# Kernel optimization log

Measured on AMD Instinct MI355X. Metric: run time of the kernel, lower is better.

Reference implementation:

```python
import jax, jax.numpy as jnp
import numpy as np

INV3 = 1.0 / np.sqrt(3.0)


def setup_inputs() -> dict:
    key = jax.random.key(0)
    ks = jax.random.split(key, 16)
    N, E = 50000, 800000
    inp = {
        'node_input': jax.random.normal(ks[0], (N, 160), jnp.float32),
        'node_attr': jnp.ones((N, 1), jnp.float32),
        'edge_attr': jax.random.normal(ks[1], (E, 4), jnp.float32),
        'edge_scalars': jax.random.normal(ks[2], (E, 8), jnp.float32),
        # params (e3nn internal weights ~ N(0,1))
        'sc_w0': jax.random.normal(ks[3], (64, 64), jnp.float32),
        'sc_w1': jax.random.normal(ks[4], (32, 32), jnp.float32),
        'lin1_w0': jax.random.normal(ks[5], (64, 64), jnp.float32),
        'lin1_w1': jax.random.normal(ks[6], (32, 32), jnp.float32),
        'fc_w1': jax.random.normal(ks[7], (8, 64), jnp.float32),
        'fc_w2': jax.random.normal(ks[8], (64, 192), jnp.float32),
        'lin2_w0': jax.random.normal(ks[9], (96, 64), jnp.float32),
        'lin2_w1': jax.random.normal(ks[10], (96, 32), jnp.float32),
        'lin3_w': jax.random.normal(ks[11], (96, 1), jnp.float32),
        'edge_src': jax.random.randint(ks[12], (E,), 0, N),
        'edge_dst': jax.random.randint(ks[13], (E,), 0, N),
        'num_neighbors': 16,
    }
    return inp


def _fctp(x_s, x_v, attr, w0, w1):
    # FullyConnectedTensorProduct(irreps, '0e', irreps-like): per-irrep linear * scalar attr,
    # path-normalized by 1/sqrt(fan_in mul)
    s = (x_s @ w0) * (1.0 / np.sqrt(x_s.shape[-1])) * attr
    v = jnp.einsum('nud,uw->nwd', x_v, w1) * (1.0 / np.sqrt(x_v.shape[-2])) * attr[..., None]
    return s, v


def reference(node_input, node_attr, edge_attr, edge_scalars,
              sc_w0, sc_w1, lin1_w0, lin1_w1, fc_w1, fc_w2,
              lin2_w0, lin2_w1, lin3_w, edge_src, edge_dst, num_neighbors):
    N = node_input.shape[0]
    # radial MLP -> per-edge TP weights [E, 192]
    h = jax.nn.silu(edge_scalars @ fc_w1 * (1.0 / np.sqrt(8.0)))
    weight = (h @ fc_w2) * (1.0 / np.sqrt(64.0))

    xs, xv = node_input[:, :64], node_input[:, 64:].reshape(N, 32, 3)  # 64x0e, 32x1o
    sc_s, sc_v = _fctp(xs, xv, node_attr, sc_w0, sc_w1)       # self connection
    f_s, f_v = _fctp(xs, xv, node_attr, lin1_w0, lin1_w1)     # lin1

    gs = f_s[edge_src]                 # [E,64]
    gv = f_v[edge_src]                 # [E,32,3]
    ys, yv = edge_attr[:, :1], edge_attr[:, 1:]  # SH 0e, 1o
    w1_, w2_ = weight[:, :64], weight[:, 64:128]
    w3_, w4_ = weight[:, 128:160], weight[:, 160:192]
    # uvu tensor-product paths (component-normalized CG)
    m0a = gs * ys * w1_                                        # 0e x 0e -> 64x0e
    m0b = jnp.sum(gv * yv[:, None, :], -1) * INV3 * w4_        # 1o x 1o -> 32x0e
    m1a = gs[..., None] * yv[:, None, :] * w2_[..., None]      # 0e x 1o -> 64x1o
    m1b = gv * ys[..., None] * w3_[..., None]                  # 1o x 0e -> 32x1o
    E = m0a.shape[0]
    edge_feat = jnp.concatenate(
        [m0a, m0b, m1a.reshape(E, 192), m1b.reshape(E, 96)], -1)  # [E,384] mid layout

    mid = jax.ops.segment_sum(edge_feat, edge_dst, num_segments=N)
    mid = mid / np.sqrt(float(num_neighbors))
    mid_s, mid_v = mid[:, :96], mid[:, 96:].reshape(N, 96, 3)

    c_s, c_v = _fctp(mid_s, mid_v, node_attr, lin2_w0, lin2_w1)
    conv = jnp.concatenate([c_s, c_v.reshape(N, -1)], -1)
    scfeat = jnp.concatenate([sc_s, sc_v.reshape(N, -1)], -1)

    angle = 0.1 * (mid_s @ lin3_w) * (1.0 / np.sqrt(96.0)) * node_attr  # [N,1]
    # sc.output_mask is all-ones here (every output irrep has a path), so sin unchanged
    return jnp.cos(angle) * scfeat + jnp.sin(angle) * conv
```

## Files before the change

kernel.cpp:

```cpp
#include <hip/hip_runtime.h>
#include <math.h>

#define INV3 0.57735026918962576f
#define RS8  0.35355339059327373f
#define RS32 0.17677669529663687f
#define RS64 0.125f
#define RS96 0.10206207261596575f
#define CAP  96

typedef _Float16 v8h   __attribute__((ext_vector_type(8)));
typedef float    f32x4 __attribute__((ext_vector_type(4)));

__global__ void node_prep(const float* __restrict__ node_input,
                          const float* __restrict__ node_attr,
                          const float* __restrict__ w0,
                          const float* __restrict__ w1,
                          float* __restrict__ f, int N) {
    int n = blockIdx.x;
    if (n >= N) return;
    __shared__ float x[160];
    int t = threadIdx.x;
    for (int i = t; i < 160; i += 64) x[i] = node_input[(size_t)n * 160 + i];
    __syncthreads();
    float attr = node_attr[n];
    float acc = 0.f;
    #pragma unroll 8
    for (int i = 0; i < 64; ++i) acc += x[i] * w0[i * 64 + t];
    f[(size_t)n * 160 + t] = acc * RS64 * attr;
    for (int o = t; o < 96; o += 64) {
        int w = o / 3, d = o % 3;
        float a = 0.f;
        #pragma unroll 8
        for (int u = 0; u < 32; ++u) a += x[64 + u * 3 + d] * w1[u * 32 + w];
        f[(size_t)n * 160 + 64 + o] = a * RS32 * attr;
    }
}

__global__ void fill_csr(const int* __restrict__ edge_dst, int* __restrict__ deg,
                         int* __restrict__ bucket, int E) {
    int e = blockIdx.x * blockDim.x + threadIdx.x;
    if (e >= E) return;
    int d = edge_dst[e];
    int pos = atomicAdd(&deg[d], 1);
    if (pos < CAP) bucket[(size_t)d * CAP + pos] = e;
}

__global__ void swizzle_w2(const float* __restrict__ fc_w2, _Float16* __restrict__ Bsw) {
    int idx = blockIdx.x * blockDim.x + threadIdx.x;
    if (idx >= 12288) return;
    int j = idx & 7;
    int l = (idx >> 3) & 63;
    int q = (idx >> 9) & 1;
    int t = idx >> 10;
    int k = q * 32 + ((l >> 4) * 8) + j;
    int n = t * 16 + (l & 15);
    Bsw[idx] = (_Float16)(fc_w2[k * 192 + n] * RS64);
}

__global__ __launch_bounds__(64, 4) void node_main(
    const float* __restrict__ node_input,
    const float* __restrict__ node_attr,
    const float* __restrict__ edge_attr,
    const float* __restrict__ edge_scalars,
    const float* __restrict__ fc_w1,
    const float* __restrict__ f,
    const _Float16* __restrict__ Bsw_g,
    const int* __restrict__ deg,
    const int* __restrict__ bucket,
    const int* __restrict__ edge_src,
    const float* __restrict__ sc_w0,
    const float* __restrict__ sc_w1,
    const float* __restrict__ lin2_w0,
    const float* __restrict__ lin2_w1,
    const float* __restrict__ lin3_w,
    const int* __restrict__ num_neighbors,
    float* __restrict__ out, int N)
{
    __shared__ __align__(16) _Float16 Hl[1024];
    __shared__ __align__(16) _Float16 Wl[16 * 208];
    __shared__ __align__(16) float    ES[16][8];
    __shared__ __align__(16) float    EA[16][4];
    __shared__ int SRC[16];

    const int lane = threadIdx.x;
    const int n    = blockIdx.x;
    if (n >= N) return;

    float fw1[8];
    #pragma unroll
    for (int u = 0; u < 8; ++u) fw1[u] = fc_w1[u * 64 + lane];

    int deg_n = min(deg[n], CAP);
    int nch = (deg_n + 15) >> 4;

    float a0 = 0.f, a1x = 0.f, a1y = 0.f, a1z = 0.f;
    float a2x = 0.f, a2y = 0.f, a2z = 0.f;
    const int m16  = lane & 15;
    const int quad = lane >> 4;
    const int wv   = lane & 31;

    for (int ch = 0; ch < nch; ++ch) {
        int vcnt = deg_n - ch * 16;
        vcnt = vcnt > 16 ? 16 : vcnt;

        if (lane < 16) {
            int i = lane;
            if (i < vcnt) {
                int e = bucket[(size_t)n * CAP + ch * 16 + i];
                SRC[i] = edge_src[e];
                *(float4*)&EA[i][0] = ((const float4*)edge_attr)[e];
                *(float4*)&ES[i][0] = ((const float4*)edge_scalars)[2 * e];
                *(float4*)&ES[i][4] = ((const float4*)edge_scalars)[2 * e + 1];
            } else {
                float4 z = make_float4(0.f, 0.f, 0.f, 0.f);
                SRC[i] = 0;
                *(float4*)&EA[i][0] = z;
                *(float4*)&ES[i][0] = z;
                *(float4*)&ES[i][4] = z;
            }
        }
        __syncthreads();

        #pragma unroll 4
        for (int i = 0; i < 16; ++i) {
            float4 e0 = *(const float4*)&ES[i][0];
            float4 e1 = *(const float4*)&ES[i][4];
            float acc = e0.x * fw1[0] + e0.y * fw1[1] + e0.z * fw1[2] + e0.w * fw1[3]
                      + e1.x * fw1[4] + e1.y * fw1[5] + e1.z * fw1[6] + e1.w * fw1[7];
            acc *= RS8;
            float hh = acc / (1.f + __expf(-acc));
            Hl[i * 64 + lane] = (_Float16)hh;
        }
        __syncthreads();

        v8h A0 = *(const v8h*)&Hl[m16 * 64 + quad * 8];
        v8h A1 = *(const v8h*)&Hl[m16 * 64 + 32 + quad * 8];
        #pragma unroll
        for (int t = 0; t < 12; ++t) {
            v8h B0 = *(const v8h*)&Bsw_g[(2 * t + 0) * 512 + lane * 8];
            v8h B1 = *(const v8h*)&Bsw_g[(2 * t + 1) * 512 + lane * 8];
            f32x4 c = {0.f, 0.f, 0.f, 0.f};
            c = __builtin_amdgcn_mfma_f32_16x16x32_f16(A0, B0, c, 0, 0, 0);
            c = __builtin_amdgcn_mfma_f32_16x16x32_f16(A1, B1, c, 0, 0, 0);
            #pragma unroll
            for (int r = 0; r < 4; ++r)
                Wl[(quad * 4 + r) * 208 + t * 16 + m16] = (_Float16)c[r];
        }
        __syncthreads();

        for (int i0 = 0; i0 < vcnt; i0 += 4) {
            float W0v[4], W1v[4], W2v[4];
            float4 eav[4];
            const float* fsv[4];
            #pragma unroll
            for (int j = 0; j < 4; ++j) {
                int i = i0 + j;
                W0v[j] = (float)Wl[i * 208 + lane];
                W1v[j] = (float)Wl[i * 208 + 64 + lane];
                W2v[j] = (float)Wl[i * 208 + 128 + lane];
                eav[j] = *(const float4*)&EA[i][0];
                fsv[j] = f + (size_t)SRC[i] * 160;
            }
            float gsv[4], g0v[4], g1v[4], g2v[4];
            #pragma unroll
            for (int j = 0; j < 4; ++j) {
                gsv[j] = fsv[j][lane];
                g0v[j] = fsv[j][64 + wv * 3 + 0];
                g1v[j] = fsv[j][64 + wv * 3 + 1];
                g2v[j] = fsv[j][64 + wv * 3 + 2];
            }
            #pragma unroll
            for (int j = 0; j < 4; ++j) {
                float4 ea = eav[j];
                a0 += gsv[j] * ea.x * W0v[j];
                float gW1 = gsv[j] * W1v[j];
                a1x += gW1 * ea.y; a1y += gW1 * ea.z; a1z += gW1 * ea.w;
                if (lane < 32) {
                    float t2 = ea.x * W2v[j];
                    a2x += g0v[j] * t2; a2y += g1v[j] * t2; a2z += g2v[j] * t2;
                } else {
                    a2x += (g0v[j] * ea.y + g1v[j] * ea.z + g2v[j] * ea.w)
                           * (INV3 * W2v[j]);
                }
            }
        }
        __syncthreads();
    }

    float* M = (float*)&Wl[0];
    float* X = (float*)&Hl[0];
    float rs = rsqrtf((float)num_neighbors[0]);
    M[lane] = a0 * rs;
    M[96 + lane * 3 + 0] = a1x * rs;
    M[96 + lane * 3 + 1] = a1y * rs;
    M[96 + lane * 3 + 2] = a1z * rs;
    if (lane < 32) {
        M[288 + lane * 3 + 0] = a2x * rs;
        M[288 + lane * 3 + 1] = a2y * rs;
        M[288 + lane * 3 + 2] = a2z * rs;
    } else {
        M[64 + (lane - 32)] = a2x * rs;
    }
    for (int i = lane; i < 160; i += 64) X[i] = node_input[(size_t)n * 160 + i];
    __syncthreads();

    float attr = node_attr[n];
    float ang = 0.f;
    #pragma unroll 8
    for (int u = 0; u < 96; ++u) ang += M[u] * lin3_w[u];
    ang *= 0.1f * RS96 * attr;
    float ca = cosf(ang), sa = sinf(ang);

    float cs = 0.f;
    #pragma unroll 8
    for (int u = 0; u < 96; ++u) cs += M[u] * lin2_w0[u * 64 + lane];
    cs *= RS96 * attr;
    float ss = 0.f;
    #pragma unroll 8
    for (int i2 = 0; i2 < 64; ++i2) ss += X[i2] * sc_w0[i2 * 64 + lane];
    ss *= RS64 * attr;
    out[(size_t)n * 160 + lane] = ca * ss + sa * cs;

    for (int o = lane; o < 96; o += 64) {
        int ww = o / 3, d = o % 3;
        float cv = 0.f;
        #pragma unroll 8
        for (int u = 0; u < 96; ++u) cv += M[96 + u * 3 + d] * lin2_w1[u * 32 + ww];
        cv *= RS96 * attr;
        float sv = 0.f;
        #pragma unroll 8
        for (int u = 0; u < 32; ++u) sv += X[64 + u * 3 + d] * sc_w1[u * 32 + ww];
        sv *= RS32 * attr;
        out[(size_t)n * 160 + 64 + o] = ca * sv + sa * cv;
    }
}

extern "C" void kernel_launch(void* const* d_in, const int* in_sizes, int n_in,
                              void* d_out, int out_size, void* d_ws, size_t ws_size,
                              hipStream_t stream) {
    const float* node_input   = (const float*)d_in[0];
    const float* node_attr    = (const float*)d_in[1];
    const float* edge_attr    = (const float*)d_in[2];
    const float* edge_scalars = (const float*)d_in[3];
    const float* sc_w0        = (const float*)d_in[4];
    const float* sc_w1        = (const float*)d_in[5];
    const float* lin1_w0      = (const float*)d_in[6];
    const float* lin1_w1      = (const float*)d_in[7];
    const float* fc_w1        = (const float*)d_in[8];
    const float* fc_w2        = (const float*)d_in[9];
    const float* lin2_w0      = (const float*)d_in[10];
    const float* lin2_w1      = (const float*)d_in[11];
    const float* lin3_w       = (const float*)d_in[12];
    const int*   edge_src     = (const int*)d_in[13];
    const int*   edge_dst     = (const int*)d_in[14];
    const int*   num_neigh    = (const int*)d_in[15];

    int N = in_sizes[0] / 160;
    int E = in_sizes[13];

    char* ws = (char*)d_ws;
    size_t off = 0;
    float* f = (float*)(ws + off);            off += ((size_t)N * 160 * 4 + 255) & ~(size_t)255;
    int* deg = (int*)(ws + off);              off += ((size_t)N * 4 + 255) & ~(size_t)255;
    int* bucket = (int*)(ws + off);           off += ((size_t)N * CAP * 4 + 255) & ~(size_t)255;
    _Float16* Bsw_g = (_Float16*)(ws + off);  off += (12288 * 2 + 255) & ~(size_t)255;

    hipMemsetAsync(deg, 0, (size_t)N * sizeof(int), stream);

    fill_csr<<<(E + 255) / 256, 256, 0, stream>>>(edge_dst, deg, bucket, E);
    swizzle_w2<<<48, 256, 0, stream>>>(fc_w2, Bsw_g);
    node_prep<<<N, 64, 0, stream>>>(node_input, node_attr, lin1_w0, lin1_w1, f, N);

    node_main<<<N, 64, 0, stream>>>(
        node_input, node_attr, edge_attr, edge_scalars, fc_w1, f, Bsw_g,
        deg, bucket, edge_src, sc_w0, sc_w1, lin2_w0, lin2_w1, lin3_w,
        num_neigh, (float*)d_out, N);
}
```

Baseline: 768.5 us.

## Batch node linear layers on MFMA and split epilogue into separate kernel

Replaces the per-node scalar linear layers (lin1 prep, and the lin2/sc/lin3 epilogue) with kernels that process 16 nodes per block using fp16 MFMA. A single swizzle kernel pre-packs all weight matrices and folds the normalization constants into them. node_main now writes fp16 mid features to a workspace buffer, which the new final kernel reads. Source-feature gathers for all 16 edges are issued before the radial MLP so their latency can overlap with it, and the per-node edge cap drops from 96 to 64. The trade-off is lower precision from fp16 inputs and the stored fp16 mid features, an extra global round-trip for mid, and a lower degree cap.

```diff
diff --git a/kernel.cpp b/kernel.cpp
--- a/kernel.cpp
+++ b/kernel.cpp
@@ -6,34 +6,49 @@
 #define RS32 0.17677669529663687f
 #define RS64 0.125f
 #define RS96 0.10206207261596575f
-#define CAP  96
+#define CAP  64
 
 typedef _Float16 v8h   __attribute__((ext_vector_type(8)));
 typedef float    f32x4 __attribute__((ext_vector_type(4)));
 
-__global__ void node_prep(const float* __restrict__ node_input,
-                          const float* __restrict__ node_attr,
-                          const float* __restrict__ w0,
-                          const float* __restrict__ w1,
-                          float* __restrict__ f, int N) {
-    int n = blockIdx.x;
-    if (n >= N) return;
-    __shared__ float x[160];
-    int t = threadIdx.x;
-    for (int i = t; i < 160; i += 64) x[i] = node_input[(size_t)n * 160 + i];
-    __syncthreads();
-    float attr = node_attr[n];
-    float acc = 0.f;
-    #pragma unroll 8
-    for (int i = 0; i < 64; ++i) acc += x[i] * w0[i * 64 + t];
-    f[(size_t)n * 160 + t] = acc * RS64 * attr;
-    for (int o = t; o < 96; o += 64) {
-        int w = o / 3, d = o % 3;
-        float a = 0.f;
-        #pragma unroll 8
-        for (int u = 0; u < 32; ++u) a += x[64 + u * 3 + d] * w1[u * 32 + w];
-        f[(size_t)n * 160 + 64 + o] = a * RS32 * attr;
-    }
+#define OFF_W2    0
+#define OFF_L2W0  12288
+#define OFF_L2W1  18432
+#define OFF_SCW0  21504
+#define OFF_SCW1  25600
+#define OFF_L1W0  26624
+#define OFF_L1W1  30720
+#define SWZ_TOTAL 31744
+
+#define MFMA16(a,b,c) __builtin_amdgcn_mfma_f32_16x16x32_f16((a),(b),(c),0,0,0)
+
+__global__ void swizzle_all(const float* __restrict__ fc_w2,
+                            const float* __restrict__ lin2_w0,
+                            const float* __restrict__ lin2_w1,
+                            const float* __restrict__ sc_w0,
+                            const float* __restrict__ sc_w1,
+                            const float* __restrict__ lin1_w0,
+                            const float* __restrict__ lin1_w1,
+                            const int* __restrict__ nn,
+                            _Float16* __restrict__ B) {
+    int idx = blockIdx.x * blockDim.x + threadIdx.x;
+    if (idx >= SWZ_TOTAL) return;
+    float rs = rsqrtf((float)nn[0]);
+    const float* W; int M, off; float s;
+    if      (idx < OFF_L2W0) { W = fc_w2;   M = 192; off = OFF_W2;   s = RS64; }
+    else if (idx < OFF_L2W1) { W = lin2_w0; M = 64;  off = OFF_L2W0; s = RS96 * rs; }
+    else if (idx < OFF_SCW0) { W = lin2_w1; M = 32;  off = OFF_L2W1; s = RS96 * rs; }
+    else if (idx < OFF_SCW1) { W = sc_w0;   M = 64;  off = OFF_SCW0; s = RS64; }
+    else if (idx < OFF_L1W0) { W = sc_w1;   M = 32;  off = OFF_SCW1; s = RS32; }
+    else if (idx < OFF_L1W1) { W = lin1_w0; M = 64;  off = OFF_L1W0; s = RS64; }
+    else                     { W = lin1_w1; M = 32;  off = OFF_L1W1; s = RS32; }
+    int rel  = idx - off;
+    int j    = rel & 7, l = (rel >> 3) & 63, frag = rel >> 9;
+    int NT   = M >> 4;
+    int nt   = frag % NT, ks = frag / NT;
+    int k    = ks * 32 + ((l >> 4) << 3) + j;
+    int n    = (nt << 4) + (l & 15);
+    B[idx] = (_Float16)(W[k * M + n] * s);
 }
 
 __global__ void fill_csr(const int* __restrict__ edge_dst, int* __restrict__ deg,
@@ -45,36 +60,70 @@
     if (pos < CAP) bucket[(size_t)d * CAP + pos] = e;
 }
 
-__global__ void swizzle_w2(const float* __restrict__ fc_w2, _Float16* __restrict__ Bsw) {
-    int idx = blockIdx.x * blockDim.x + threadIdx.x;
-    if (idx >= 12288) return;
-    int j = idx & 7;
-    int l = (idx >> 3) & 63;
-    int q = (idx >> 9) & 1;
-    int t = idx >> 10;
-    int k = q * 32 + ((l >> 4) * 8) + j;
-    int n = t * 16 + (l & 15);
-    Bsw[idx] = (_Float16)(fc_w2[k * 192 + n] * RS64);
+__global__ __launch_bounds__(64) void prep_mfma(
+    const float* __restrict__ ni, const float* __restrict__ na,
+    const _Float16* __restrict__ Bsw, float* __restrict__ fout, int N)
+{
+    __shared__ __align__(16) _Float16 Xs[16][72];
+    __shared__ __align__(16) _Float16 Xv[3][16][40];
+    __shared__ float At[16];
+    const int lane = threadIdx.x;
+    const int n0 = blockIdx.x * 16;
+    const int j1 = lane + 64, j2 = lane + 128;
+    _Float16* xd1 = &Xv[(j1 - 64) % 3][0][(j1 - 64) / 3];
+    _Float16* xd2 = (lane < 32) ? &Xv[(j2 - 64) % 3][0][(j2 - 64) / 3] : (_Float16*)0;
+    for (int m = 0; m < 16; ++m) {
+        const float* row = ni + (size_t)min(n0 + m, N - 1) * 160;
+        Xs[m][lane] = (_Float16)row[lane];
+        xd1[m * 40] = (_Float16)row[j1];
+        if (lane < 32) xd2[m * 40] = (_Float16)row[j2];
+    }
+    if (lane < 16) At[lane] = na[min(n0 + lane, N - 1)];
+    __syncthreads();
+
+    const int m16 = lane & 15, quad = lane >> 4;
+    v8h A0 = *(const v8h*)&Xs[m16][quad * 8];
+    v8h A1 = *(const v8h*)&Xs[m16][32 + quad * 8];
+    const _Float16* B0 = Bsw + OFF_L1W0;
+    #pragma unroll
+    for (int nt = 0; nt < 4; ++nt) {
+        f32x4 c = {0.f, 0.f, 0.f, 0.f};
+        c = MFMA16(A0, *(const v8h*)&B0[(0 * 4 + nt) * 512 + lane * 8], c);
+        c = MFMA16(A1, *(const v8h*)&B0[(1 * 4 + nt) * 512 + lane * 8], c);
+        #pragma unroll
+        for (int r = 0; r < 4; ++r) {
+            int rr = quad * 4 + r, n = n0 + rr;
+            if (n < N) fout[(size_t)n * 160 + nt * 16 + m16] = c[r] * At[rr];
+        }
+    }
+    const _Float16* B1 = Bsw + OFF_L1W1;
+    #pragma unroll
+    for (int d = 0; d < 3; ++d) {
+        v8h Ad = *(const v8h*)&Xv[d][m16][quad * 8];
+        #pragma unroll
+        for (int nt = 0; nt < 2; ++nt) {
+            f32x4 c = {0.f, 0.f, 0.f, 0.f};
+            c = MFMA16(Ad, *(const v8h*)&B1[nt * 512 + lane * 8], c);
+            #pragma unroll
+            for (int r = 0; r < 4; ++r) {
+                int rr = quad * 4 + r, n = n0 + rr;
+                if (n < N) fout[(size_t)n * 160 + 64 + (nt * 16 + m16) * 3 + d] = c[r] * At[rr];
+            }
+        }
+    }
 }
 
 __global__ __launch_bounds__(64, 4) void node_main(
-    const float* __restrict__ node_input,
-    const float* __restrict__ node_attr,
     const float* __restrict__ edge_attr,
     const float* __restrict__ edge_scalars,
     const float* __restrict__ fc_w1,
     const float* __restrict__ f,
-    const _Float16* __restrict__ Bsw_g,
+    const _Float16* __restrict__ Bsw,
     const int* __restrict__ deg,
     const int* __restrict__ bucket,
     const int* __restrict__ edge_src,
-    const float* __restrict__ sc_w0,
-    const float* __restrict__ sc_w1,
-    const float* __restrict__ lin2_w0,
-    const float* __restrict__ lin2_w1,
-    const float* __restrict__ lin3_w,
-    const int* __restrict__ num_neighbors,
-    float* __restrict__ out, int N)
+    _Float16* __restrict__ mid16,
+    int N)
 {
     __shared__ __align__(16) _Float16 Hl[1024];
     __shared__ __align__(16) _Float16 Wl[16 * 208];
@@ -98,6 +147,8 @@
     const int m16  = lane & 15;
     const int quad = lane >> 4;
     const int wv   = lane & 31;
+    const int wv3  = 64 + wv * 3;
+    const _Float16* Bw2 = Bsw + OFF_W2;
 
     for (int ch = 0; ch < nch; ++ch) {
         int vcnt = deg_n - ch * 16;
@@ -121,6 +172,16 @@
         }
         __syncthreads();
 
+        float gs[16], g0[16], g1[16], g2[16];
+        #pragma unroll
+        for (int i = 0; i < 16; ++i) {
+            const float* fs = f + (size_t)SRC[i] * 160;
+            gs[i] = fs[lane];
+            g0[i] = fs[wv3 + 0];
+            g1[i] = fs[wv3 + 1];
+            g2[i] = fs[wv3 + 2];
+        }
+
         #pragma unroll 4
         for (int i = 0; i < 16; ++i) {
             float4 e0 = *(const float4*)&ES[i][0];
@@ -128,8 +189,7 @@
             float acc = e0.x * fw1[0] + e0.y * fw1[1] + e0.z * fw1[2] + e0.w * fw1[3]
                       + e1.x * fw1[4] + e1.y * fw1[5] + e1.z * fw1[6] + e1.w * fw1[7];
             acc *= RS8;
-            float hh = acc / (1.f + __expf(-acc));
-            Hl[i * 64 + lane] = (_Float16)hh;
+            Hl[i * 64 + lane] = (_Float16)(acc / (1.f + __expf(-acc)));
         }
         __syncthreads();
 
@@ -137,101 +197,149 @@
         v8h A1 = *(const v8h*)&Hl[m16 * 64 + 32 + quad * 8];
         #pragma unroll
         for (int t = 0; t < 12; ++t) {
-            v8h B0 = *(const v8h*)&Bsw_g[(2 * t + 0) * 512 + lane * 8];
-            v8h B1 = *(const v8h*)&Bsw_g[(2 * t + 1) * 512 + lane * 8];
+            v8h B0 = *(const v8h*)&Bw2[(0 * 12 + t) * 512 + lane * 8];
+            v8h B1 = *(const v8h*)&Bw2[(1 * 12 + t) * 512 + lane * 8];
             f32x4 c = {0.f, 0.f, 0.f, 0.f};
-            c = __builtin_amdgcn_mfma_f32_16x16x32_f16(A0, B0, c, 0, 0, 0);
-            c = __builtin_amdgcn_mfma_f32_16x16x32_f16(A1, B1, c, 0, 0, 0);
+            c = MFMA16(A0, B0, c);
+            c = MFMA16(A1, B1, c);
             #pragma unroll
             for (int r = 0; r < 4; ++r)
                 Wl[(quad * 4 + r) * 208 + t * 16 + m16] = (_Float16)c[r];
         }
         __syncthreads();
 
-        for (int i0 = 0; i0 < vcnt; i0 += 4) {
-            float W0v[4], W1v[4], W2v[4];
-            float4 eav[4];
-            const float* fsv[4];
+        #pragma unroll 4
+        for (int i = 0; i < 16; ++i) {
+            float W0 = (float)Wl[i * 208 + lane];
+            float W1 = (float)Wl[i * 208 + 64 + lane];
+            float W2 = (float)Wl[i * 208 + 128 + lane];
+            float4 ea = *(const float4*)&EA[i][0];
+            a0 += gs[i] * ea.x * W0;
+            float gW1 = gs[i] * W1;
+            a1x += gW1 * ea.y; a1y += gW1 * ea.z; a1z += gW1 * ea.w;
+            if (lane < 32) {
+                float t2 = ea.x * W2;
+                a2x += g0[i] * t2; a2y += g1[i] * t2; a2z += g2[i] * t2;
+            } else {
+                a2x += (g0[i] * ea.y + g1[i] * ea.z + g2[i] * ea.w)
+                       * (INV3 * W2);
+            }
+        }
+        __syncthreads();
+    }
+
+    _Float16* md = mid16 + (size_t)n * 384;
+    md[lane] = (_Float16)a0;
+    md[96 + lane * 3 + 0] = (_Float16)a1x;
+    md[96 + lane * 3 + 1] = (_Float16)a1y;
+    md[96 + lane * 3 + 2] = (_Float16)a1z;
+    if (lane < 32) {
+        md[288 + wv * 3 + 0] = (_Float16)a2x;
+        md[288 + wv * 3 + 1] = (_Float16)a2y;
+        md[288 + wv * 3 + 2] = (_Float16)a2z;
+    } else {
+        md[64 + wv] = (_Float16)a2x;
+    }
+}
+
+__global__ __launch_bounds__(64) void final_mfma(
+    const float* __restrict__ ni, const float* __restrict__ na,
+    const _Float16* __restrict__ mid16, const _Float16* __restrict__ Bsw,
+    const float* __restrict__ lin3_w, const int* __restrict__ nn,
+    float* __restrict__ out, int N)
+{
+    __shared__ __align__(16) _Float16 Ms[16][104];
+    __shared__ __align__(16) _Float16 Mv[3][16][104];
+    __shared__ __align__(16) _Float16 Xs[16][72];
+    __shared__ __align__(16) _Float16 Xv[3][16][40];
+    __shared__ float At[16], CA[16], SA[16];
+    const int lane = threadIdx.x;
+    const int n0 = blockIdx.x * 16;
+
+    _Float16* mdst[6];
+    #pragma unroll
+    for (int t = 0; t < 6; ++t) {
+        int j = lane + t * 64;
+        mdst[t] = (j < 96) ? &Ms[0][j] : &Mv[(j - 96) % 3][0][(j - 96) / 3];
+    }
+    for (int m = 0; m < 16; ++m) {
+        const _Float16* row = mid16 + (size_t)min(n0 + m, N - 1) * 384;
+        #pragma unroll
+        for (int t = 0; t < 6; ++t) mdst[t][m * 104] = row[lane + t * 64];
+    }
+    const int j1 = lane + 64, j2 = lane + 128;
+    _Float16* xd1 = &Xv[(j1 - 64) % 3][0][(j1 - 64) / 3];
+    _Float16* xd2 = (lane < 32) ? &Xv[(j2 - 64) % 3][0][(j2 - 64) / 3] : (_Float16*)0;
+    for (int m = 0; m < 16; ++m) {
+        const float* row = ni + (size_t)min(n0 + m, N - 1) * 160;
+        Xs[m][lane] = (_Float16)row[lane];
+        xd1[m * 40] = (_Float16)row[j1];
+        if (lane < 32) xd2[m * 40] = (_Float16)row[j2];
+    }
+    if (lane < 16) At[lane] = na[min(n0 + lane, N - 1)];
+    __syncthreads();
+
+    if (lane < 16) {
+        float rs = rsqrtf((float)nn[0]);
+        float ang = 0.f;
+        #pragma unroll 8
+        for (int k = 0; k < 96; ++k) ang += (float)Ms[lane][k] * lin3_w[k];
+        ang *= 0.1f * RS96 * rs * At[lane];
+        CA[lane] = cosf(ang);
+        SA[lane] = sinf(ang);
+    }
+    __syncthreads();
+
+    const int m16 = lane & 15, quad = lane >> 4;
+    v8h As[3], Ax0, Ax1;
+    #pragma unroll
+    for (int ks = 0; ks < 3; ++ks) As[ks] = *(const v8h*)&Ms[m16][ks * 32 + quad * 8];
+    Ax0 = *(const v8h*)&Xs[m16][quad * 8];
+    Ax1 = *(const v8h*)&Xs[m16][32 + quad * 8];
+
+    const _Float16* Bl2w0 = Bsw + OFF_L2W0;
+    const _Float16* Bscw0 = Bsw + OFF_SCW0;
+    #pragma unroll
+    for (int nt = 0; nt < 4; ++nt) {
+        f32x4 c = {0.f, 0.f, 0.f, 0.f};
+        #pragma unroll
+        for (int ks = 0; ks < 3; ++ks)
+            c = MFMA16(As[ks], *(const v8h*)&Bl2w0[(ks * 4 + nt) * 512 + lane * 8], c);
+        f32x4 s = {0.f, 0.f, 0.f, 0.f};
+        s = MFMA16(Ax0, *(const v8h*)&Bscw0[(0 * 4 + nt) * 512 + lane * 8], s);
+        s = MFMA16(Ax1, *(const v8h*)&Bscw0[(1 * 4 + nt) * 512 + lane * 8], s);
+        #pragma unroll
+        for (int r = 0; r < 4; ++r) {
+            int rr = quad * 4 + r, n = n0 + rr;
+            if (n < N)
+                out[(size_t)n * 160 + nt * 16 + m16] =
+                    At[rr] * (CA[rr] * s[r] + SA[rr] * c[r]);
+        }
+    }
+    const _Float16* Bl2w1 = Bsw + OFF_L2W1;
+    const _Float16* Bscw1 = Bsw + OFF_SCW1;
+    #pragma unroll
+    for (int d = 0; d < 3; ++d) {
+        v8h Am0 = *(const v8h*)&Mv[d][m16][0 * 32 + quad * 8];
+        v8h Am1 = *(const v8h*)&Mv[d][m16][1 * 32 + quad * 8];
+        v8h Am2 = *(const v8h*)&Mv[d][m16][2 * 32 + quad * 8];
+        v8h Axv = *(const v8h*)&Xv[d][m16][quad * 8];
+        #pragma unroll
+        for (int nt = 0; nt < 2; ++nt) {
+            f32x4 c = {0.f, 0.f, 0.f, 0.f};
+            c = MFMA16(Am0, *(const v8h*)&Bl2w1[(0 * 2 + nt) * 512 + lane * 8], c);
+            c = MFMA16(Am1, *(const v8h*)&Bl2w1[(1 * 2 + nt) * 512 + lane * 8], c);
+            c = MFMA16(Am2, *(const v8h*)&Bl2w1[(2 * 2 + nt) * 512 + lane * 8], c);
+            f32x4 s = {0.f, 0.f, 0.f, 0.f};
+            s = MFMA16(Axv, *(const v8h*)&Bscw1[nt * 512 + lane * 8], s);
             #pragma unroll
-            for (int j = 0; j < 4; ++j) {
-                int i = i0 + j;
-                W0v[j] = (float)Wl[i * 208 + lane];
-                W1v[j] = (float)Wl[i * 208 + 64 + lane];
-                W2v[j] = (float)Wl[i * 208 + 128 + lane];
-                eav[j] = *(const float4*)&EA[i][0];
-                fsv[j] = f + (size_t)SRC[i] * 160;
+            for (int r = 0; r < 4; ++r) {
+                int rr = quad * 4 + r, n = n0 + rr;
+                if (n < N)
+                    out[(size_t)n * 160 + 64 + (nt * 16 + m16) * 3 + d] =
+                        At[rr] * (CA[rr] * s[r] + SA[rr] * c[r]);
             }
-            float gsv[4], g0v[4], g1v[4], g2v[4];
-            #pragma unroll
-            for (int j = 0; j < 4; ++j) {
-                gsv[j] = fsv[j][lane];
-                g0v[j] = fsv[j][64 + wv * 3 + 0];
-                g1v[j] = fsv[j][64 + wv * 3 + 1];
-                g2v[j] = fsv[j][64 + wv * 3 + 2];
-            }
-            #pragma unroll
-            for (int j = 0; j < 4; ++j) {
-                float4 ea = eav[j];
-                a0 += gsv[j] * ea.x * W0v[j];
-                float gW1 = gsv[j] * W1v[j];
-                a1x += gW1 * ea.y; a1y += gW1 * ea.z; a1z += gW1 * ea.w;
-                if (lane < 32) {
-                    float t2 = ea.x * W2v[j];
-                    a2x += g0v[j] * t2; a2y += g1v[j] * t2; a2z += g2v[j] * t2;
-                } else {
-                    a2x += (g0v[j] * ea.y + g1v[j] * ea.z + g2v[j] * ea.w)
-                           * (INV3 * W2v[j]);
-                }
-            }
-        }
-        __syncthreads();
-    }
-
-    float* M = (float*)&Wl[0];
-    float* X = (float*)&Hl[0];
-    float rs = rsqrtf((float)num_neighbors[0]);
-    M[lane] = a0 * rs;
-    M[96 + lane * 3 + 0] = a1x * rs;
-    M[96 + lane * 3 + 1] = a1y * rs;
-    M[96 + lane * 3 + 2] = a1z * rs;
-    if (lane < 32) {
-        M[288 + lane * 3 + 0] = a2x * rs;
-        M[288 + lane * 3 + 1] = a2y * rs;
-        M[288 + lane * 3 + 2] = a2z * rs;
-    } else {
-        M[64 + (lane - 32)] = a2x * rs;
-    }
-    for (int i = lane; i < 160; i += 64) X[i] = node_input[(size_t)n * 160 + i];
-    __syncthreads();
-
-    float attr = node_attr[n];
-    float ang = 0.f;
-    #pragma unroll 8
-    for (int u = 0; u < 96; ++u) ang += M[u] * lin3_w[u];
-    ang *= 0.1f * RS96 * attr;
-    float ca = cosf(ang), sa = sinf(ang);
-
-    float cs = 0.f;
-    #pragma unroll 8
-    for (int u = 0; u < 96; ++u) cs += M[u] * lin2_w0[u * 64 + lane];
-    cs *= RS96 * attr;
-    float ss = 0.f;
-    #pragma unroll 8
-    for (int i2 = 0; i2 < 64; ++i2) ss += X[i2] * sc_w0[i2 * 64 + lane];
-    ss *= RS64 * attr;
-    out[(size_t)n * 160 + lane] = ca * ss + sa * cs;
-
-    for (int o = lane; o < 96; o += 64) {
-        int ww = o / 3, d = o % 3;
-        float cv = 0.f;
-        #pragma unroll 8
-        for (int u = 0; u < 96; ++u) cv += M[96 + u * 3 + d] * lin2_w1[u * 32 + ww];
-        cv *= RS96 * attr;
-        float sv = 0.f;
-        #pragma unroll 8
-        for (int u = 0; u < 32; ++u) sv += X[64 + u * 3 + d] * sc_w1[u * 32 + ww];
-        sv *= RS32 * attr;
-        out[(size_t)n * 160 + 64 + o] = ca * sv + sa * cv;
+        }
     }
 }
 
@@ -263,16 +371,19 @@
     float* f = (float*)(ws + off);            off += ((size_t)N * 160 * 4 + 255) & ~(size_t)255;
     int* deg = (int*)(ws + off);              off += ((size_t)N * 4 + 255) & ~(size_t)255;
     int* bucket = (int*)(ws + off);           off += ((size_t)N * CAP * 4 + 255) & ~(size_t)255;
-    _Float16* Bsw_g = (_Float16*)(ws + off);  off += (12288 * 2 + 255) & ~(size_t)255;
+    _Float16* mid16 = (_Float16*)(ws + off);  off += ((size_t)N * 384 * 2 + 255) & ~(size_t)255;
+    _Float16* Bsw = (_Float16*)(ws + off);    off += (SWZ_TOTAL * 2 + 255) & ~(size_t)255;
 
     hipMemsetAsync(deg, 0, (size_t)N * sizeof(int), stream);
 
     fill_csr<<<(E + 255) / 256, 256, 0, stream>>>(edge_dst, deg, bucket, E);
-    swizzle_w2<<<48, 256, 0, stream>>>(fc_w2, Bsw_g);
-    node_prep<<<N, 64, 0, stream>>>(node_input, node_attr, lin1_w0, lin1_w1, f, N);
-
-    node_main<<<N, 64, 0, stream>>>(
-        node_input, node_attr, edge_attr, edge_scalars, fc_w1, f, Bsw_g,
-        deg, bucket, edge_src, sc_w0, sc_w1, lin2_w0, lin2_w1, lin3_w,
-        num_neigh, (float*)d_out, N);
-}
+    swizzle_all<<<(SWZ_TOTAL + 255) / 256, 256, 0, stream>>>(
+        fc_w2, lin2_w0, lin2_w1, sc_w0, sc_w1, lin1_w0, lin1_w1, num_neigh, Bsw);
+    prep_mfma<<<(N + 15) / 16, 64, 0, stream>>>(node_input, node_attr, Bsw, f, N);
+
+    node_main<<<N, 64, 0, stream>>>(edge_attr, edge_scalars, fc_w1, f, Bsw,
+                                    deg, bucket, edge_src, mid16, N);
+
+    final_mfma<<<(N + 15) / 16, 64, 0, stream>>>(node_input, node_attr, mid16, Bsw,
+                                                 lin3_w, num_neigh, (float*)d_out, N);
+}
```

Result: slower. 875.1 us (+13.9%).
